# Kernel tuning notes

Hardware: AMD Instinct MI355X
Metric: run time of the kernel (lower is better)

The kernel has to match this reference:

```python
import jax, jax.numpy as jnp
import numpy as np

SB_EPSILON = 0.1
SB_SIZE = 1

B, S, L = 16, 256, 24


def _shift(x, axis, k):
    """y[..., i, ...] = x[..., i + k, ...], zero-padded out of range."""
    if k == 0:
        return x
    n = x.shape[axis]
    if k > 0:
        body = jax.lax.slice_in_dim(x, k, n, axis=axis)
        pad = jnp.zeros_like(jax.lax.slice_in_dim(x, 0, k, axis=axis))
        return jnp.concatenate([body, pad], axis=axis)
    k = -k
    body = jax.lax.slice_in_dim(x, 0, n - k, axis=axis)
    pad = jnp.zeros_like(jax.lax.slice_in_dim(x, 0, k, axis=axis))
    return jnp.concatenate([pad, body], axis=axis)


def setup_inputs() -> dict:
    key = jax.random.key(0)
    k1, k2 = jax.random.split(key)
    predict = jax.random.normal(k1, (B, S, S, L), dtype=jnp.float32)
    target = (jax.random.uniform(k2, (B, S, S, L)) < 0.002).astype(jnp.float32)
    # valid spans: end >= start
    tri = (jnp.arange(S)[None, :] >= jnp.arange(S)[:, None]).astype(jnp.int32)
    mask = jnp.broadcast_to(tri[None, :, :, None], (B, S, S, L)).astype(jnp.int32)
    # keep targets only on valid spans
    target = target * mask.astype(jnp.float32)
    return {"predict": predict, "target": target, "mask": mask}


def reference(predict, target, mask):
    dt = predict.dtype
    P = (target == 1).astype(dt)            # positive spans [B,S,S,L]
    M = (mask == 1).astype(dt)              # valid-span mask
    # subtract full epsilon from each positive span
    b2l = jnp.where(target == 1, target - SB_EPSILON, target)
    for dist in range(1, SB_SIZE + 1):
        eps = SB_EPSILON / (SB_SIZE * dist * 4)
        cnt = jnp.zeros_like(P)   # num valid neighbors per positive span
        add = jnp.zeros_like(P)   # smoothing mass scattered onto neighbors
        # NOTE: original code offsets neighbors by sb_size (not dist); identical for sb_size=1
        for axis, k in ((2, SB_SIZE), (2, -SB_SIZE), (1, SB_SIZE), (1, -SB_SIZE)):
            cnt = cnt + _shift(M, axis, k)          # neighbor in range and mask==1
            add = add + _shift(P, axis, -k)         # positives scattering into this cell
        b2l = b2l + eps * (add * M + P * (dist * 4 - cnt))
    # masked BCE-with-logits, mean over mask==1 elements
    x, t = predict, b2l
    bce = jnp.maximum(x, 0) - x * t + jnp.log1p(jnp.exp(-jnp.abs(x)))
    denom = jnp.sum(M)
    return jnp.sum(bce * M) / denom
```

## Files before the change

### kernel.cpp

```cpp
#include <hip/hip_runtime.h>


#define SS 256
#define LL 24

constexpr float EPS4      = 0.025f;
constexpr float INV_DENOM = 1.0f / 12632064.0f;
constexpr int   NT        = 256;
constexpr int   NB        = 16 * 128;
constexpr int   TOTAL6    = 257 * 6;
constexpr float LOG2E     = 1.4426950408889634f;
constexpr float LN2       = 0.6931471805599453f;

__device__ __forceinline__ float sp_part(float x) {
    float u = __builtin_amdgcn_exp2f(-LOG2E * fabsf(x));
    return fmaxf(x, 0.f) + LN2 * __builtin_amdgcn_logf(1.f + u);
}

__global__ __launch_bounds__(NT) void bs_pair(const float4* __restrict__ pred4,
                                              const uint4*  __restrict__ targ4,
                                              const float*  __restrict__ predf,
                                              float* __restrict__ partial) {
    const int b  = blockIdx.x >> 7;
    const int iA = blockIdx.x & 127;
    const int iB = 255 - iA;
    const int lenA6 = (SS - iA) * 6;
    const int qA = (((b << 8) + iA) * SS + iA) * 6;
    const int qB = (((b << 8) + iB) * SS + iB) * 6;

    float acc  = 0.f;
    float corr = 0.f;

    int v = threadIdx.x;
    int q = (v < lenA6) ? (qA + v) : (qB + (v - lenA6));
    float4 x = pred4[q];
    uint4  t = targ4[q];

    for (;;) {
        int  vn = v + NT;
        bool more = vn < TOTAL6;
        int qn = 0; float4 xn; uint4 tn;
        if (more) {
            qn = (vn < lenA6) ? (qA + vn) : (qB + (vn - lenA6));
            xn = pred4[qn];
            tn = targ4[qn];
        }

        acc += sp_part(x.x) + sp_part(x.y) + sp_part(x.z) + sp_part(x.w);

        if ((t.x | t.y | t.z | t.w) != 0u) {
            int vloc = (v < lenA6) ? v : (v - lenA6);
            int i    = (v < lenA6) ? iA : iB;
            int j    = i + vloc / 6;
            bool hasL = j > i;
            bool hasR = j < SS - 1;
            bool hasU = i > 0;
            float cnt = (hasL ? 2.f : 0.f) + (hasR ? 1.f : 0.f) + (hasU ? 1.f : 0.f);
            int ebase = q * 4;
            unsigned tu[4] = {t.x, t.y, t.z, t.w};
            float    xv[4] = {x.x, x.y, x.z, x.w};
#pragma unroll
            for (int k = 0; k < 4; ++k) {
                if (tu[k] != 0u) {
                    int e = ebase + k;
                    float s = 0.f;
                    if (hasL) s += predf[e - LL];
                    if (hasR) s += predf[e + LL];
                    if (hasU) s += predf[e - LL * SS];
                    if (hasL) s += predf[e + LL * SS];
                    corr += fmaf(EPS4, s - xv[k] * cnt, xv[k]);
                }
            }
        }

        if (!more) break;
        v = vn; q = qn; x = xn; t = tn;
    }

    float vsum = acc - corr;

#pragma unroll
    for (int off = 32; off; off >>= 1) vsum += __shfl_down(vsum, off, 64);
    __shared__ float s[NT / 64];
    int w = threadIdx.x >> 6;
    if ((threadIdx.x & 63) == 0) s[w] = vsum;
    __syncthreads();
    if (threadIdx.x == 0) {
        float bsum = 0.f;
#pragma unroll
        for (int k = 0; k < NT / 64; ++k) bsum += s[k];
        partial[blockIdx.x] = bsum;
    }
}

__global__ __launch_bounds__(256) void bs_final(const float* __restrict__ partial,
                                                float* __restrict__ out) {
    float acc = 0.f;
#pragma unroll
    for (int k = threadIdx.x; k < NB; k += 256) acc += partial[k];
#pragma unroll
    for (int off = 32; off; off >>= 1) acc += __shfl_down(acc, off, 64);
    __shared__ float s[4];
    int w = threadIdx.x >> 6;
    if ((threadIdx.x & 63) == 0) s[w] = acc;
    __syncthreads();
    if (threadIdx.x == 0)
        out[0] = (s[0] + s[1] + s[2] + s[3]) * INV_DENOM;
}

extern "C" void kernel_launch(void* const* d_in, const int* in_sizes, int n_in,
                              void* d_out, int out_size, void* d_ws, size_t ws_size,
                              hipStream_t stream) {
    const float4* pred4 = (const float4*)d_in[0];
    const uint4*  targ4 = (const uint4*)d_in[1];
    const float*  predf = (const float*)d_in[0];
    float* partial = (float*)d_ws;
    float* out     = (float*)d_out;

    bs_pair <<<NB, NT, 0, stream>>>(pred4, targ4, predf, partial);
    bs_final<<<1, 256, 0, stream>>>(partial, out);
}
```

Baseline: 238.3 us.

## Stream the full rectangle with a grid-stride unrolled loop and triangle masking

Replaces the per-row-pair triangular traversal with a flat grid-stride sweep over the whole B×S×S×L tensor. Each of 12 fully unrolled iterations issues nontemporal vector loads, and lower-triangle cells are dropped with a j>=i select instead of being skipped. The aim is simpler indexing and more independent loads in flight to raise memory-level parallelism. The cost is reading and evaluating the softplus on roughly twice the data, since the invalid half of the tensor is now loaded and computed too.

```diff
diff --git a/kernel.cpp b/kernel.cpp
--- a/kernel.cpp
+++ b/kernel.cpp
@@ -4,59 +4,56 @@
 #define SS 256
 #define LL 24
 
-constexpr float EPS4      = 0.025f;
-constexpr float INV_DENOM = 1.0f / 12632064.0f;
-constexpr int   NT        = 256;
-constexpr int   NB        = 16 * 128;
-constexpr int   TOTAL6    = 257 * 6;
-constexpr float LOG2E     = 1.4426950408889634f;
-constexpr float LN2       = 0.6931471805599453f;
+typedef float    fvec4 __attribute__((ext_vector_type(4)));
+typedef unsigned uvec4 __attribute__((ext_vector_type(4)));
+
+constexpr float    EPS4      = 0.025f;
+constexpr float    INV_DENOM = 1.0f / 12632064.0f;
+constexpr int      NT        = 256;
+constexpr int      NB        = 2048;
+constexpr unsigned NV4       = 16u * 256u * 256u * 6u;
+constexpr unsigned STRIDE    = (unsigned)(NB * NT);
+constexpr int      NITER     = (int)(NV4 / STRIDE);
+constexpr float    LOG2E     = 1.4426950408889634f;
+constexpr float    LN2       = 0.6931471805599453f;
 
 __device__ __forceinline__ float sp_part(float x) {
     float u = __builtin_amdgcn_exp2f(-LOG2E * fabsf(x));
     return fmaxf(x, 0.f) + LN2 * __builtin_amdgcn_logf(1.f + u);
 }
 
-__global__ __launch_bounds__(NT) void bs_pair(const float4* __restrict__ pred4,
-                                              const uint4*  __restrict__ targ4,
-                                              const float*  __restrict__ predf,
+__device__ __forceinline__ float sp4(const fvec4& x) {
+    return sp_part(x.x) + sp_part(x.y) + sp_part(x.z) + sp_part(x.w);
+}
+
+__global__ __launch_bounds__(NT) void bs_rect(const fvec4* __restrict__ pred4,
+                                              const uvec4* __restrict__ targ4,
+                                              const float* __restrict__ predf,
                                               float* __restrict__ partial) {
-    const int b  = blockIdx.x >> 7;
-    const int iA = blockIdx.x & 127;
-    const int iB = 255 - iA;
-    const int lenA6 = (SS - iA) * 6;
-    const int qA = (((b << 8) + iA) * SS + iA) * 6;
-    const int qB = (((b << 8) + iB) * SS + iB) * 6;
-
+    const unsigned gid = blockIdx.x * NT + threadIdx.x;
     float acc  = 0.f;
     float corr = 0.f;
 
-    int v = threadIdx.x;
-    int q = (v < lenA6) ? (qA + v) : (qB + (v - lenA6));
-    float4 x = pred4[q];
-    uint4  t = targ4[q];
+#pragma unroll
+    for (int it = 0; it < NITER; ++it) {
+        unsigned q = gid + (unsigned)it * STRIDE;
 
-    for (;;) {
-        int  vn = v + NT;
-        bool more = vn < TOTAL6;
-        int qn = 0; float4 xn; uint4 tn;
-        if (more) {
-            qn = (vn < lenA6) ? (qA + vn) : (qB + (vn - lenA6));
-            xn = pred4[qn];
-            tn = targ4[qn];
-        }
+        fvec4 x = __builtin_nontemporal_load(pred4 + q);
+        uvec4 t = __builtin_nontemporal_load(targ4 + q);
 
-        acc += sp_part(x.x) + sp_part(x.y) + sp_part(x.z) + sp_part(x.w);
+        unsigned cell = q / 6u;
+        int j = (int)(cell & 255u);
+        int i = (int)((cell >> 8) & 255u);
+
+        float s4 = sp4(x);
+        acc += (j >= i) ? s4 : 0.f;
 
         if ((t.x | t.y | t.z | t.w) != 0u) {
-            int vloc = (v < lenA6) ? v : (v - lenA6);
-            int i    = (v < lenA6) ? iA : iB;
-            int j    = i + vloc / 6;
             bool hasL = j > i;
             bool hasR = j < SS - 1;
             bool hasU = i > 0;
             float cnt = (hasL ? 2.f : 0.f) + (hasR ? 1.f : 0.f) + (hasU ? 1.f : 0.f);
-            int ebase = q * 4;
+            int ebase = (int)q * 4;
             unsigned tu[4] = {t.x, t.y, t.z, t.w};
             float    xv[4] = {x.x, x.y, x.z, x.w};
 #pragma unroll
@@ -72,9 +69,6 @@
                 }
             }
         }
-
-        if (!more) break;
-        v = vn; q = qn; x = xn; t = tn;
     }
 
     float vsum = acc - corr;
@@ -111,12 +105,12 @@
 extern "C" void kernel_launch(void* const* d_in, const int* in_sizes, int n_in,
                               void* d_out, int out_size, void* d_ws, size_t ws_size,
                               hipStream_t stream) {
-    const float4* pred4 = (const float4*)d_in[0];
-    const uint4*  targ4 = (const uint4*)d_in[1];
-    const float*  predf = (const float*)d_in[0];
+    const fvec4* pred4 = (const fvec4*)d_in[0];
+    const uvec4* targ4 = (const uvec4*)d_in[1];
+    const float* predf = (const float*)d_in[0];
     float* partial = (float*)d_ws;
     float* out     = (float*)d_out;
 
-    bs_pair <<<NB, NT, 0, stream>>>(pred4, targ4, predf, partial);
+    bs_rect <<<NB, NT, 0, stream>>>(pred4, targ4, predf, partial);
     bs_final<<<1, 256, 0, stream>>>(partial, out);
 }
```

Result: slower. 259.0 us (+8.7%).
